# Kernel tuning notes

Measured on AMD Instinct MI355X. Metric: run time of the kernel, lower is better.

## Reference

```python
import jax, jax.numpy as jnp
import numpy as np

HEAD_SIZE = 64   # baseChn * max_channel_ratio
NUM_HEADS = 2
LEAKY_ALPHA = 0.3  # tf.keras.layers.LeakyReLU default


def setup_inputs() -> dict:
    key = jax.random.key(0)
    ks = jax.random.split(key, 6)
    x = jax.random.normal(ks[0], (96, 48, 512), dtype=jnp.float32)
    y = jax.random.uniform(ks[1], (96, 64, 64), dtype=jnp.float32)
    nItem = jax.random.uniform(ks[2], (96,), dtype=jnp.float32, minval=1.0, maxval=48.0)
    W_proj = jax.random.normal(ks[3], (512, 64), dtype=jnp.float32) * 0.05
    W1 = jax.random.normal(ks[4], (64, 128), dtype=jnp.float32) * 0.1
    W2 = jax.random.normal(ks[5], (2, 1), dtype=jnp.float32)
    return {"x": x, "y": y, "nItem": nItem, "W_proj": W_proj, "W1": W1, "W2": W2}


def reference(x, y, nItem, W_proj, W1, W2):
    # fc_cnn_proj: Dense(64, gelu exact, no bias)
    gallery = jax.nn.gelu(jnp.matmul(x, W_proj), approximate=False)  # [Sx, Nx, 64]
    Sx, Nx, _ = gallery.shape
    Sy, Ny, _ = y.shape
    sqrt_hs = jnp.sqrt(jnp.float32(HEAD_SIZE))
    # shared linear (no bias) then split heads: [S, H, N, hs]
    px = jnp.matmul(gallery, W1).reshape(Sx, Nx, NUM_HEADS, HEAD_SIZE).transpose(0, 2, 1, 3)
    py = jnp.matmul(y, W1).reshape(Sy, Ny, NUM_HEADS, HEAD_SIZE).transpose(0, 2, 1, 3)
    # pairwise cross-set attention maps: [Sy, Sx, H, Ny, Nx]
    att = jnp.einsum('yhmd,xhnd->yxhmn', py, px) / sqrt_hs
    att = jnp.where(att > 0, att, LEAKY_ALPHA * att)
    # reduce over both item axes, normalize by nItem[x] and nItemMax_y
    sc = att.sum(axis=(3, 4)) / nItem[None, :, None] / jnp.float32(Ny)  # [Sy, Sx, H]
    scores = jnp.matmul(sc, W2)  # linear2: Dense(1, no bias) -> [Sy, Sx, 1]
    return scores
```

## Files before the change

### kernel.cpp

```cpp
#include <hip/hip_runtime.h>
#include <hip/hip_bf16.h>


typedef short bf16x8 __attribute__((ext_vector_type(8)));
typedef float f32x4 __attribute__((ext_vector_type(4)));

__device__ __forceinline__ unsigned short f2bf(float v) {
  __hip_bfloat16 b = __float2bfloat16(v);
  return *reinterpret_cast<unsigned short*>(&b);
}

__device__ __forceinline__ bf16x8 load8_cvt(const float* __restrict__ p) {
  f32x4 v0 = *reinterpret_cast<const f32x4*>(p);
  f32x4 v1 = *reinterpret_cast<const f32x4*>(p + 4);
  bf16x8 r;
  r[0] = (short)f2bf(v0[0]); r[1] = (short)f2bf(v0[1]);
  r[2] = (short)f2bf(v0[2]); r[3] = (short)f2bf(v0[3]);
  r[4] = (short)f2bf(v1[0]); r[5] = (short)f2bf(v1[1]);
  r[6] = (short)f2bf(v1[2]); r[7] = (short)f2bf(v1[3]);
  return r;
}

__global__ __launch_bounds__(256) void k_wprep(const float* __restrict__ Wp,
                                               const float* __restrict__ W1,
                                               unsigned short* __restrict__ WpF,
                                               unsigned short* __restrict__ W1F) {
  int tid = blockIdx.x * 256 + threadIdx.x;
  if (tid < 32768) {
    int kc = tid >> 11, nt = (tid >> 9) & 3, l = (tid >> 3) & 63, i = tid & 7;
    int k = 32 * kc + 8 * (l >> 4) + i, c = nt * 16 + (l & 15);
    WpF[tid] = f2bf(Wp[k * 64 + c]);
  } else {
    int t2 = tid - 32768;
    int kc = t2 >> 12, nt = (t2 >> 9) & 7, l = (t2 >> 3) & 63, i = t2 & 7;
    int k = 32 * kc + 8 * (l >> 4) + i, d = nt * 16 + (l & 15);
    W1F[t2] = f2bf(W1[k * 128 + d]);
  }
}

__global__ __launch_bounds__(256) void k_py(const float* __restrict__ y,
                                            const unsigned short* __restrict__ W1F_u,
                                            unsigned short* __restrict__ pyf) {
  int lane = threadIdx.x & 63;
  int w = threadIdx.x >> 6;
  int T = blockIdx.x * 4 + w;
  const bf16x8* W1F = reinterpret_cast<const bf16x8*>(W1F_u);
  const float* yb = y + (size_t)(T * 16 + (lane & 15)) * 64 + 8 * (lane >> 4);
  bf16x8 a0 = load8_cvt(yb);
  bf16x8 a1 = load8_cvt(yb + 32);
  f32x4 acc[8];
#pragma unroll
  for (int nt = 0; nt < 8; ++nt) acc[nt] = (f32x4){0.f, 0.f, 0.f, 0.f};
#pragma unroll
  for (int nt = 0; nt < 8; ++nt) {
    acc[nt] = __builtin_amdgcn_mfma_f32_16x16x32_bf16(a0, W1F[nt * 64 + lane], acc[nt], 0, 0, 0);
    acc[nt] = __builtin_amdgcn_mfma_f32_16x16x32_bf16(a1, W1F[(8 + nt) * 64 + lane], acc[nt], 0, 0, 0);
  }
  int r_hi = (lane >> 4) * 4;
#pragma unroll
  for (int nt = 0; nt < 8; ++nt) {
    int d = nt * 16 + (lane & 15);
    int h = d >> 6, dd = d & 63;
    int kc = dd >> 5, q = (dd >> 3) & 3, i = dd & 7;
#pragma unroll
    for (int j = 0; j < 4; ++j) {
      int row = T * 16 + r_hi + j;
      int yi = row >> 6, m = row & 63;
      int mt = m >> 4, rr = m & 15;
      size_t idx = ((size_t)((yi * 2 + h) * 8 + mt * 2 + kc)) * 512 + (rr + (q << 4)) * 8 + i;
      pyf[idx] = f2bf(acc[nt][j]);
    }
  }
}

__global__ __launch_bounds__(256) void k_gal_px(const float* __restrict__ x,
                                                const unsigned short* __restrict__ WpF_u,
                                                const unsigned short* __restrict__ W1F_u,
                                                unsigned short* __restrict__ pxf) {
  __shared__ float red[4 * 16 * 64];
  __shared__ unsigned short gal[16 * 72];
  int lane = threadIdx.x & 63;
  int w = threadIdx.x >> 6;
  int rowbase = blockIdx.x * 16;
  const bf16x8* WpF = reinterpret_cast<const bf16x8*>(WpF_u);
  const bf16x8* W1F = reinterpret_cast<const bf16x8*>(W1F_u);
  const float* xb = x + (size_t)(rowbase + (lane & 15)) * 512 + 8 * (lane >> 4);

  f32x4 acc1[4];
#pragma unroll
  for (int nt = 0; nt < 4; ++nt) acc1[nt] = (f32x4){0.f, 0.f, 0.f, 0.f};
#pragma unroll
  for (int kk = 0; kk < 4; ++kk) {
    int kc = w * 4 + kk;
    bf16x8 a = load8_cvt(xb + 32 * kc);
#pragma unroll
    for (int nt = 0; nt < 4; ++nt)
      acc1[nt] = __builtin_amdgcn_mfma_f32_16x16x32_bf16(a, WpF[(kc * 4 + nt) * 64 + lane], acc1[nt], 0, 0, 0);
  }
#pragma unroll
  for (int nt = 0; nt < 4; ++nt)
#pragma unroll
    for (int j = 0; j < 4; ++j)
      red[(w * 16 + nt * 4 + j) * 64 + lane] = acc1[nt][j];
  __syncthreads();
#pragma unroll
  for (int j = 0; j < 4; ++j) {
    float s = red[(0 * 16 + w * 4 + j) * 64 + lane] + red[(1 * 16 + w * 4 + j) * 64 + lane]
            + red[(2 * 16 + w * 4 + j) * 64 + lane] + red[(3 * 16 + w * 4 + j) * 64 + lane];
    float ge = 0.5f * s * (1.0f + erff(s * 0.70710678118654752f));
    int r = (lane >> 4) * 4 + j;
    int c = w * 16 + (lane & 15);
    gal[r * 72 + c] = f2bf(ge);
  }
  __syncthreads();
  const unsigned short* gp = &gal[(lane & 15) * 72 + 8 * (lane >> 4)];
  bf16x8 g0 = *reinterpret_cast<const bf16x8*>(gp);
  bf16x8 g1 = *reinterpret_cast<const bf16x8*>(gp + 32);
  f32x4 acc2[2];
  acc2[0] = (f32x4){0.f, 0.f, 0.f, 0.f};
  acc2[1] = (f32x4){0.f, 0.f, 0.f, 0.f};
#pragma unroll
  for (int u = 0; u < 2; ++u) {
    int nt = w * 2 + u;
    acc2[u] = __builtin_amdgcn_mfma_f32_16x16x32_bf16(g0, W1F[nt * 64 + lane], acc2[u], 0, 0, 0);
    acc2[u] = __builtin_amdgcn_mfma_f32_16x16x32_bf16(g1, W1F[(8 + nt) * 64 + lane], acc2[u], 0, 0, 0);
  }
#pragma unroll
  for (int u = 0; u < 2; ++u) {
    int nt = w * 2 + u;
    int d = nt * 16 + (lane & 15);
    int h = d >> 6, dd = d & 63;
    int kc = dd >> 5, q = (dd >> 3) & 3, i = dd & 7;
#pragma unroll
    for (int j = 0; j < 4; ++j) {
      int row = rowbase + (lane >> 4) * 4 + j;
      int xi = row / 48, n = row % 48;
      int nt3 = n >> 4, rr = n & 15;
      size_t idx = ((size_t)((xi * 2 + h) * 6 + nt3 * 2 + kc)) * 512 + (rr + (q << 4)) * 8 + i;
      pxf[idx] = f2bf(acc2[u][j]);
    }
  }
}

__global__ __launch_bounds__(256) void k_att(const unsigned short* __restrict__ pyf_u,
                                             const unsigned short* __restrict__ pxf_u,
                                             const float* __restrict__ nItem,
                                             const float* __restrict__ W2,
                                             float* __restrict__ out) {
  int lane = threadIdx.x & 63;
  int w = threadIdx.x >> 6;
  int yi = blockIdx.x / 6;
  int xib = (blockIdx.x % 6) * 16 + w * 4;
  const bf16x8* PA = reinterpret_cast<const bf16x8*>(pyf_u);
  const bf16x8* PB = reinterpret_cast<const bf16x8*>(pxf_u);
  float sv[4][2];
#pragma unroll
  for (int g = 0; g < 4; ++g) { sv[g][0] = 0.f; sv[g][1] = 0.f; }
#pragma unroll
  for (int h = 0; h < 2; ++h) {
    bf16x8 a[4][2];
    size_t ab = (size_t)(yi * 2 + h) * 512 + lane;
#pragma unroll
    for (int mt = 0; mt < 4; ++mt) {
      a[mt][0] = PA[ab + (mt * 2 + 0) * 64];
      a[mt][1] = PA[ab + (mt * 2 + 1) * 64];
    }
#pragma unroll
    for (int g = 0; g < 4; ++g) {
      size_t bb = (size_t)((xib + g) * 2 + h) * 384 + lane;
      bf16x8 b[3][2];
#pragma unroll
      for (int nt = 0; nt < 3; ++nt) {
        b[nt][0] = PB[bb + (nt * 2 + 0) * 64];
        b[nt][1] = PB[bb + (nt * 2 + 1) * 64];
      }
      float sz = 0.f, sr = 0.f;
#pragma unroll
      for (int nt = 0; nt < 3; ++nt)
#pragma unroll
        for (int mt = 0; mt < 4; ++mt) {
          f32x4 acc = {0.f, 0.f, 0.f, 0.f};
          acc = __builtin_amdgcn_mfma_f32_16x16x32_bf16(a[mt][0], b[nt][0], acc, 0, 0, 0);
          acc = __builtin_amdgcn_mfma_f32_16x16x32_bf16(a[mt][1], b[nt][1], acc, 0, 0, 0);
#pragma unroll
          for (int j = 0; j < 4; ++j) { sz += acc[j]; sr += fmaxf(acc[j], 0.f); }
        }
      sv[g][h] += 0.3f * sz + 0.7f * sr;
    }
  }
#pragma unroll
  for (int g = 0; g < 4; ++g)
#pragma unroll
    for (int h = 0; h < 2; ++h)
#pragma unroll
      for (int off = 32; off >= 1; off >>= 1)
        sv[g][h] += __shfl_xor(sv[g][h], off, 64);
  if (lane == 0) {
    float w2a = W2[0], w2b = W2[1];
#pragma unroll
    for (int g = 0; g < 4; ++g) {
      int xi = xib + g;
      out[yi * 96 + xi] = (sv[g][0] * w2a + sv[g][1] * w2b) / (512.0f * nItem[xi]);
    }
  }
}

extern "C" void kernel_launch(void* const* d_in, const int* in_sizes, int n_in,
                              void* d_out, int out_size, void* d_ws, size_t ws_size,
                              hipStream_t stream) {
  const float* x     = (const float*)d_in[0];
  const float* y     = (const float*)d_in[1];
  const float* nItem = (const float*)d_in[2];
  const float* Wp    = (const float*)d_in[3];
  const float* W1    = (const float*)d_in[4];
  const float* W2    = (const float*)d_in[5];
  float* out = (float*)d_out;

  unsigned short* WpF = (unsigned short*)d_ws;
  unsigned short* W1F = WpF + 32768;
  unsigned short* pyf = W1F + 8192;
  unsigned short* pxf = pyf + 786432;

  hipLaunchKernelGGL(k_wprep, dim3(160), dim3(256), 0, stream, Wp, W1, WpF, W1F);
  hipLaunchKernelGGL(k_py, dim3(96), dim3(256), 0, stream, y, W1F, pyf);
  hipLaunchKernelGGL(k_gal_px, dim3(288), dim3(256), 0, stream, x, WpF, W1F, pxf);
  hipLaunchKernelGGL(k_att, dim3(576), dim3(256), 0, stream, pyf, pxf, nItem, W2, out);
}
```

Baseline: 40.81 us.

## Fuse weight prep, py and gallery/px projections into one kernel; restructure attention

Merges the weight-reformatting, py projection and gallery/px projection kernels into a single launch. Each block converts W1 and W_proj to bf16 fragment layout in shared memory, so the separate prep kernel and its global round-trip go away. Each wave now runs the full K=512 gallery GEMM itself instead of reducing partial sums across waves through LDS. The attention kernel is remapped so each wave owns one y-row with all of its A fragments held in registers, and W2 and the leaky-ReLU constants are folded into vector accumulators. The cost is that every block repeats the weight conversion, and there are fewer, heavier blocks (72 for x).

New measurement: 34.89 us. 14.5% less time.

```diff
diff --git a/kernel.cpp b/kernel.cpp
--- a/kernel.cpp
+++ b/kernel.cpp
@@ -21,123 +21,134 @@
   return r;
 }
 
-__global__ __launch_bounds__(256) void k_wprep(const float* __restrict__ Wp,
-                                               const float* __restrict__ W1,
-                                               unsigned short* __restrict__ WpF,
-                                               unsigned short* __restrict__ W1F) {
-  int tid = blockIdx.x * 256 + threadIdx.x;
-  if (tid < 32768) {
-    int kc = tid >> 11, nt = (tid >> 9) & 3, l = (tid >> 3) & 63, i = tid & 7;
-    int k = 32 * kc + 8 * (l >> 4) + i, c = nt * 16 + (l & 15);
-    WpF[tid] = f2bf(Wp[k * 64 + c]);
+__global__ __launch_bounds__(256) void k_prep(const float* __restrict__ x,
+                                              const float* __restrict__ y,
+                                              const float* __restrict__ Wp,
+                                              const float* __restrict__ W1,
+                                              unsigned short* __restrict__ pyf,
+                                              unsigned short* __restrict__ pxf) {
+  __shared__ unsigned short w1f[8192];
+  __shared__ unsigned short wpf[16384];
+  __shared__ unsigned short gal[4][1152];
+  int t = threadIdx.x;
+  int lane = t & 63, w = t >> 6;
+
+#pragma unroll
+  for (int it = 0; it < 32; ++it) {
+    int idx = it * 256 + t;
+    int k = idx >> 7, d = idx & 127;
+    int l = (d & 15) + 16 * ((k >> 3) & 3);
+    int f = (k >> 5) * 8 + (d >> 4);
+    w1f[f * 512 + l * 8 + (k & 7)] = f2bf(W1[idx]);
+  }
+
+  if (blockIdx.x >= 72) {
+    __syncthreads();
+    int yi = blockIdx.x - 72;
+    const bf16x8* WF = reinterpret_cast<const bf16x8*>(w1f);
+    int row0 = yi * 64 + w * 16 + (lane & 15);
+    const float* yb = y + (size_t)row0 * 64 + 8 * (lane >> 4);
+    bf16x8 a0 = load8_cvt(yb);
+    bf16x8 a1 = load8_cvt(yb + 32);
+    f32x4 acc[8];
+#pragma unroll
+    for (int nt = 0; nt < 8; ++nt) acc[nt] = (f32x4){0.f, 0.f, 0.f, 0.f};
+#pragma unroll
+    for (int nt = 0; nt < 8; ++nt) {
+      acc[nt] = __builtin_amdgcn_mfma_f32_16x16x32_bf16(a0, WF[nt * 64 + lane], acc[nt], 0, 0, 0);
+      acc[nt] = __builtin_amdgcn_mfma_f32_16x16x32_bf16(a1, WF[(8 + nt) * 64 + lane], acc[nt], 0, 0, 0);
+    }
+    int r_hi = (lane >> 4) * 4;
+#pragma unroll
+    for (int nt = 0; nt < 8; ++nt) {
+      int d = nt * 16 + (lane & 15);
+      int h = d >> 6, dd = d & 63;
+      int kc = dd >> 5, q = (dd >> 3) & 3, i = dd & 7;
+#pragma unroll
+      for (int j = 0; j < 4; ++j) {
+        int m = w * 16 + r_hi + j;
+        int mt = m >> 4, rr = m & 15;
+        size_t idx = ((size_t)((yi * 2 + h) * 8 + mt * 2 + kc)) * 512 + (rr + (q << 4)) * 8 + i;
+        pyf[idx] = f2bf(acc[nt][j]);
+      }
+    }
   } else {
-    int t2 = tid - 32768;
-    int kc = t2 >> 12, nt = (t2 >> 9) & 7, l = (t2 >> 3) & 63, i = t2 & 7;
-    int k = 32 * kc + 8 * (l >> 4) + i, d = nt * 16 + (l & 15);
-    W1F[t2] = f2bf(W1[k * 128 + d]);
-  }
-}
-
-__global__ __launch_bounds__(256) void k_py(const float* __restrict__ y,
-                                            const unsigned short* __restrict__ W1F_u,
-                                            unsigned short* __restrict__ pyf) {
-  int lane = threadIdx.x & 63;
-  int w = threadIdx.x >> 6;
-  int T = blockIdx.x * 4 + w;
-  const bf16x8* W1F = reinterpret_cast<const bf16x8*>(W1F_u);
-  const float* yb = y + (size_t)(T * 16 + (lane & 15)) * 64 + 8 * (lane >> 4);
-  bf16x8 a0 = load8_cvt(yb);
-  bf16x8 a1 = load8_cvt(yb + 32);
-  f32x4 acc[8];
-#pragma unroll
-  for (int nt = 0; nt < 8; ++nt) acc[nt] = (f32x4){0.f, 0.f, 0.f, 0.f};
-#pragma unroll
-  for (int nt = 0; nt < 8; ++nt) {
-    acc[nt] = __builtin_amdgcn_mfma_f32_16x16x32_bf16(a0, W1F[nt * 64 + lane], acc[nt], 0, 0, 0);
-    acc[nt] = __builtin_amdgcn_mfma_f32_16x16x32_bf16(a1, W1F[(8 + nt) * 64 + lane], acc[nt], 0, 0, 0);
-  }
-  int r_hi = (lane >> 4) * 4;
-#pragma unroll
-  for (int nt = 0; nt < 8; ++nt) {
-    int d = nt * 16 + (lane & 15);
-    int h = d >> 6, dd = d & 63;
-    int kc = dd >> 5, q = (dd >> 3) & 3, i = dd & 7;
-#pragma unroll
-    for (int j = 0; j < 4; ++j) {
-      int row = T * 16 + r_hi + j;
-      int yi = row >> 6, m = row & 63;
-      int mt = m >> 4, rr = m & 15;
-      size_t idx = ((size_t)((yi * 2 + h) * 8 + mt * 2 + kc)) * 512 + (rr + (q << 4)) * 8 + i;
-      pyf[idx] = f2bf(acc[nt][j]);
-    }
-  }
-}
-
-__global__ __launch_bounds__(256) void k_gal_px(const float* __restrict__ x,
-                                                const unsigned short* __restrict__ WpF_u,
-                                                const unsigned short* __restrict__ W1F_u,
-                                                unsigned short* __restrict__ pxf) {
-  __shared__ float red[4 * 16 * 64];
-  __shared__ unsigned short gal[16 * 72];
-  int lane = threadIdx.x & 63;
-  int w = threadIdx.x >> 6;
-  int rowbase = blockIdx.x * 16;
-  const bf16x8* WpF = reinterpret_cast<const bf16x8*>(WpF_u);
-  const bf16x8* W1F = reinterpret_cast<const bf16x8*>(W1F_u);
-  const float* xb = x + (size_t)(rowbase + (lane & 15)) * 512 + 8 * (lane >> 4);
-
-  f32x4 acc1[4];
-#pragma unroll
-  for (int nt = 0; nt < 4; ++nt) acc1[nt] = (f32x4){0.f, 0.f, 0.f, 0.f};
-#pragma unroll
-  for (int kk = 0; kk < 4; ++kk) {
-    int kc = w * 4 + kk;
-    bf16x8 a = load8_cvt(xb + 32 * kc);
+    int rowbase = blockIdx.x * 64;
+#pragma unroll
+    for (int it = 0; it < 64; ++it) {
+      int idx = it * 256 + t;
+      int k = idx >> 6, c = idx & 63;
+      int l = (c & 15) + 16 * ((k >> 3) & 3);
+      int g = ((k >> 5) & 7) * 4 + (c >> 4);
+      wpf[g * 512 + l * 8 + (k & 7)] = f2bf(Wp[idx]);
+    }
+    __syncthreads();
+    const bf16x8* WPF = reinterpret_cast<const bf16x8*>(wpf);
+    const bf16x8* WF = reinterpret_cast<const bf16x8*>(w1f);
+    int rloc = rowbase + w * 16 + (lane & 15);
+    const float* xb = x + (size_t)rloc * 512 + 8 * (lane >> 4);
+    f32x4 acc1[4];
+#pragma unroll
+    for (int nt = 0; nt < 4; ++nt) acc1[nt] = (f32x4){0.f, 0.f, 0.f, 0.f};
+#pragma unroll
+    for (int kc = 0; kc < 8; ++kc) {
+      bf16x8 a = load8_cvt(xb + 32 * kc);
+#pragma unroll
+      for (int nt = 0; nt < 4; ++nt)
+        acc1[nt] = __builtin_amdgcn_mfma_f32_16x16x32_bf16(a, WPF[(kc * 4 + nt) * 64 + lane], acc1[nt], 0, 0, 0);
+    }
+    __syncthreads();
+#pragma unroll
+    for (int it = 0; it < 64; ++it) {
+      int idx = it * 256 + t;
+      int k = idx >> 6, c = idx & 63;
+      int l = (c & 15) + 16 * ((k >> 3) & 3);
+      int g = ((k >> 5) & 7) * 4 + (c >> 4);
+      wpf[g * 512 + l * 8 + (k & 7)] = f2bf(Wp[16384 + idx]);
+    }
+    __syncthreads();
+#pragma unroll
+    for (int kc = 0; kc < 8; ++kc) {
+      bf16x8 a = load8_cvt(xb + 256 + 32 * kc);
+#pragma unroll
+      for (int nt = 0; nt < 4; ++nt)
+        acc1[nt] = __builtin_amdgcn_mfma_f32_16x16x32_bf16(a, WPF[(kc * 4 + nt) * 64 + lane], acc1[nt], 0, 0, 0);
+    }
 #pragma unroll
     for (int nt = 0; nt < 4; ++nt)
-      acc1[nt] = __builtin_amdgcn_mfma_f32_16x16x32_bf16(a, WpF[(kc * 4 + nt) * 64 + lane], acc1[nt], 0, 0, 0);
-  }
-#pragma unroll
-  for (int nt = 0; nt < 4; ++nt)
-#pragma unroll
-    for (int j = 0; j < 4; ++j)
-      red[(w * 16 + nt * 4 + j) * 64 + lane] = acc1[nt][j];
-  __syncthreads();
-#pragma unroll
-  for (int j = 0; j < 4; ++j) {
-    float s = red[(0 * 16 + w * 4 + j) * 64 + lane] + red[(1 * 16 + w * 4 + j) * 64 + lane]
-            + red[(2 * 16 + w * 4 + j) * 64 + lane] + red[(3 * 16 + w * 4 + j) * 64 + lane];
-    float ge = 0.5f * s * (1.0f + erff(s * 0.70710678118654752f));
-    int r = (lane >> 4) * 4 + j;
-    int c = w * 16 + (lane & 15);
-    gal[r * 72 + c] = f2bf(ge);
-  }
-  __syncthreads();
-  const unsigned short* gp = &gal[(lane & 15) * 72 + 8 * (lane >> 4)];
-  bf16x8 g0 = *reinterpret_cast<const bf16x8*>(gp);
-  bf16x8 g1 = *reinterpret_cast<const bf16x8*>(gp + 32);
-  f32x4 acc2[2];
-  acc2[0] = (f32x4){0.f, 0.f, 0.f, 0.f};
-  acc2[1] = (f32x4){0.f, 0.f, 0.f, 0.f};
-#pragma unroll
-  for (int u = 0; u < 2; ++u) {
-    int nt = w * 2 + u;
-    acc2[u] = __builtin_amdgcn_mfma_f32_16x16x32_bf16(g0, W1F[nt * 64 + lane], acc2[u], 0, 0, 0);
-    acc2[u] = __builtin_amdgcn_mfma_f32_16x16x32_bf16(g1, W1F[(8 + nt) * 64 + lane], acc2[u], 0, 0, 0);
-  }
-#pragma unroll
-  for (int u = 0; u < 2; ++u) {
-    int nt = w * 2 + u;
-    int d = nt * 16 + (lane & 15);
-    int h = d >> 6, dd = d & 63;
-    int kc = dd >> 5, q = (dd >> 3) & 3, i = dd & 7;
-#pragma unroll
-    for (int j = 0; j < 4; ++j) {
-      int row = rowbase + (lane >> 4) * 4 + j;
-      int xi = row / 48, n = row % 48;
-      int nt3 = n >> 4, rr = n & 15;
-      size_t idx = ((size_t)((xi * 2 + h) * 6 + nt3 * 2 + kc)) * 512 + (rr + (q << 4)) * 8 + i;
-      pxf[idx] = f2bf(acc2[u][j]);
+#pragma unroll
+      for (int j = 0; j < 4; ++j) {
+        float s = acc1[nt][j];
+        float ge = 0.5f * s * (1.0f + erff(s * 0.70710678118654752f));
+        int rl = (lane >> 4) * 4 + j;
+        int c = nt * 16 + (lane & 15);
+        gal[w][rl * 72 + c] = f2bf(ge);
+      }
+    const unsigned short* gp = &gal[w][(lane & 15) * 72 + 8 * (lane >> 4)];
+    bf16x8 g0 = *reinterpret_cast<const bf16x8*>(gp);
+    bf16x8 g1 = *reinterpret_cast<const bf16x8*>(gp + 32);
+    f32x4 acc2[8];
+#pragma unroll
+    for (int nt = 0; nt < 8; ++nt) acc2[nt] = (f32x4){0.f, 0.f, 0.f, 0.f};
+#pragma unroll
+    for (int nt = 0; nt < 8; ++nt) {
+      acc2[nt] = __builtin_amdgcn_mfma_f32_16x16x32_bf16(g0, WF[nt * 64 + lane], acc2[nt], 0, 0, 0);
+      acc2[nt] = __builtin_amdgcn_mfma_f32_16x16x32_bf16(g1, WF[(8 + nt) * 64 + lane], acc2[nt], 0, 0, 0);
+    }
+    int r_hi = (lane >> 4) * 4;
+#pragma unroll
+    for (int nt = 0; nt < 8; ++nt) {
+      int d = nt * 16 + (lane & 15);
+      int h = d >> 6, dd = d & 63;
+      int kc = dd >> 5, q = (dd >> 3) & 3, i = dd & 7;
+#pragma unroll
+      for (int j = 0; j < 4; ++j) {
+        int row = rowbase + w * 16 + r_hi + j;
+        int xi = row / 48, n = row % 48;
+        int nt3 = n >> 4, rr = n & 15;
+        size_t idx = ((size_t)((xi * 2 + h) * 6 + nt3 * 2 + kc)) * 512 + (rr + (q << 4)) * 8 + i;
+        pxf[idx] = f2bf(acc2[nt][j]);
+      }
     }
   }
 }
@@ -149,58 +160,58 @@
                                              float* __restrict__ out) {
   int lane = threadIdx.x & 63;
   int w = threadIdx.x >> 6;
-  int yi = blockIdx.x / 6;
-  int xib = (blockIdx.x % 6) * 16 + w * 4;
+  int yi = (blockIdx.x / 24) * 4 + w;
+  int xb = (blockIdx.x % 24) * 4;
   const bf16x8* PA = reinterpret_cast<const bf16x8*>(pyf_u);
   const bf16x8* PB = reinterpret_cast<const bf16x8*>(pxf_u);
-  float sv[4][2];
-#pragma unroll
-  for (int g = 0; g < 4; ++g) { sv[g][0] = 0.f; sv[g][1] = 0.f; }
-#pragma unroll
-  for (int h = 0; h < 2; ++h) {
-    bf16x8 a[4][2];
-    size_t ab = (size_t)(yi * 2 + h) * 512 + lane;
-#pragma unroll
-    for (int mt = 0; mt < 4; ++mt) {
-      a[mt][0] = PA[ab + (mt * 2 + 0) * 64];
-      a[mt][1] = PA[ab + (mt * 2 + 1) * 64];
-    }
+
+  f32x4 zero4 = {0.f, 0.f, 0.f, 0.f};
+  asm volatile("" : "+v"(zero4));
+
+  bf16x8 a[16];
+  size_t abase = (size_t)(yi * 2) * 512 + lane;
+#pragma unroll
+  for (int f = 0; f < 8; ++f) {
+    a[f]     = PA[abase + f * 64];
+    a[8 + f] = PA[abase + 512 + f * 64];
+  }
+  float w2h0 = W2[0], w2h1 = W2[1];
+  float res[4];
+#pragma unroll
+  for (int g = 0; g < 4; ++g) {
+    int xi = xb + g;
+    f32x4 szw = {0.f, 0.f, 0.f, 0.f};
+    f32x4 srw = {0.f, 0.f, 0.f, 0.f};
+#pragma unroll
+    for (int h = 0; h < 2; ++h) {
+      size_t bbase = (size_t)((xi * 2 + h) * 6) * 64 + lane;
+      bf16x8 b[6];
+#pragma unroll
+      for (int f = 0; f < 6; ++f) b[f] = PB[bbase + f * 64];
+      float c3 = 0.3f * (h ? w2h1 : w2h0);
+      float c7 = 0.7f * (h ? w2h1 : w2h0);
+#pragma unroll
+      for (int nt = 0; nt < 3; ++nt)
+#pragma unroll
+        for (int mt = 0; mt < 4; ++mt) {
+          f32x4 acc = __builtin_amdgcn_mfma_f32_16x16x32_bf16(a[h * 8 + mt * 2], b[nt * 2], zero4, 0, 0, 0);
+          acc = __builtin_amdgcn_mfma_f32_16x16x32_bf16(a[h * 8 + mt * 2 + 1], b[nt * 2 + 1], acc, 0, 0, 0);
+          f32x4 mx = {fmaxf(acc[0], 0.f), fmaxf(acc[1], 0.f), fmaxf(acc[2], 0.f), fmaxf(acc[3], 0.f)};
+          szw += acc * c3;
+          srw += mx * c7;
+        }
+    }
+    f32x4 t4 = szw + srw;
+    float tot = (t4[0] + t4[1]) + (t4[2] + t4[3]);
+#pragma unroll
+    for (int off = 32; off >= 1; off >>= 1) tot += __shfl_xor(tot, off, 64);
+    res[g] = tot;
+  }
+  if (lane == 0) {
 #pragma unroll
     for (int g = 0; g < 4; ++g) {
-      size_t bb = (size_t)((xib + g) * 2 + h) * 384 + lane;
-      bf16x8 b[3][2];
-#pragma unroll
-      for (int nt = 0; nt < 3; ++nt) {
-        b[nt][0] = PB[bb + (nt * 2 + 0) * 64];
-        b[nt][1] = PB[bb + (nt * 2 + 1) * 64];
-      }
-      float sz = 0.f, sr = 0.f;
-#pragma unroll
-      for (int nt = 0; nt < 3; ++nt)
-#pragma unroll
-        for (int mt = 0; mt < 4; ++mt) {
-          f32x4 acc = {0.f, 0.f, 0.f, 0.f};
-          acc = __builtin_amdgcn_mfma_f32_16x16x32_bf16(a[mt][0], b[nt][0], acc, 0, 0, 0);
-          acc = __builtin_amdgcn_mfma_f32_16x16x32_bf16(a[mt][1], b[nt][1], acc, 0, 0, 0);
-#pragma unroll
-          for (int j = 0; j < 4; ++j) { sz += acc[j]; sr += fmaxf(acc[j], 0.f); }
-        }
-      sv[g][h] += 0.3f * sz + 0.7f * sr;
-    }
-  }
-#pragma unroll
-  for (int g = 0; g < 4; ++g)
-#pragma unroll
-    for (int h = 0; h < 2; ++h)
-#pragma unroll
-      for (int off = 32; off >= 1; off >>= 1)
-        sv[g][h] += __shfl_xor(sv[g][h], off, 64);
-  if (lane == 0) {
-    float w2a = W2[0], w2b = W2[1];
-#pragma unroll
-    for (int g = 0; g < 4; ++g) {
-      int xi = xib + g;
-      out[yi * 96 + xi] = (sv[g][0] * w2a + sv[g][1] * w2b) / (512.0f * nItem[xi]);
+      int xi = xb + g;
+      out[yi * 96 + xi] = res[g] / (512.0f * nItem[xi]);
     }
   }
 }
@@ -216,13 +227,9 @@
   const float* W2    = (const float*)d_in[5];
   float* out = (float*)d_out;
 
-  unsigned short* WpF = (unsigned short*)d_ws;
-  unsigned short* W1F = WpF + 32768;
-  unsigned short* pyf = W1F + 8192;
+  unsigned short* pyf = (unsigned short*)d_ws;
   unsigned short* pxf = pyf + 786432;
 
-  hipLaunchKernelGGL(k_wprep, dim3(160), dim3(256), 0, stream, Wp, W1, WpF, W1F);
-  hipLaunchKernelGGL(k_py, dim3(96), dim3(256), 0, stream, y, W1F, pyf);
-  hipLaunchKernelGGL(k_gal_px, dim3(288), dim3(256), 0, stream, x, WpF, W1F, pxf);
+  hipLaunchKernelGGL(k_prep, dim3(168), dim3(256), 0, stream, x, y, Wp, W1, pyf, pxf);
   hipLaunchKernelGGL(k_att, dim3(576), dim3(256), 0, stream, pyf, pxf, nItem, W2, out);
 }
```

## Fuse projection, py/px computation and attention scoring into one mega kernel

Applied to the files above, without the earlier changes.

Replaces the three kernels k_py, k_gal_px and k_att with a single k_mega launched over 1152 blocks. Each block handles 4 y-sets and 2 x-sets. It recomputes the gallery projection, GELU and px for its x-sets, and py for its y-sets, keeping everything in shared memory so the pyf/pxf global round trips and two launches go away. In exchange, gallery/px work is recomputed 24 times over and py work 48 times over, which adds a large amount of redundant MFMA and global x/y reads. Wave utilization is also uneven, since only waves 0-1 handle the second x tile.

Result: slower. 86.97 us (+113.1%).

```diff
diff --git a/kernel.cpp b/kernel.cpp
--- a/kernel.cpp
+++ b/kernel.cpp
@@ -38,170 +38,170 @@
   }
 }
 
-__global__ __launch_bounds__(256) void k_py(const float* __restrict__ y,
-                                            const unsigned short* __restrict__ W1F_u,
-                                            unsigned short* __restrict__ pyf) {
-  int lane = threadIdx.x & 63;
-  int w = threadIdx.x >> 6;
-  int T = blockIdx.x * 4 + w;
-  const bf16x8* W1F = reinterpret_cast<const bf16x8*>(W1F_u);
-  const float* yb = y + (size_t)(T * 16 + (lane & 15)) * 64 + 8 * (lane >> 4);
-  bf16x8 a0 = load8_cvt(yb);
-  bf16x8 a1 = load8_cvt(yb + 32);
-  f32x4 acc[8];
-#pragma unroll
-  for (int nt = 0; nt < 8; ++nt) acc[nt] = (f32x4){0.f, 0.f, 0.f, 0.f};
-#pragma unroll
-  for (int nt = 0; nt < 8; ++nt) {
-    acc[nt] = __builtin_amdgcn_mfma_f32_16x16x32_bf16(a0, W1F[nt * 64 + lane], acc[nt], 0, 0, 0);
-    acc[nt] = __builtin_amdgcn_mfma_f32_16x16x32_bf16(a1, W1F[(8 + nt) * 64 + lane], acc[nt], 0, 0, 0);
-  }
-  int r_hi = (lane >> 4) * 4;
-#pragma unroll
-  for (int nt = 0; nt < 8; ++nt) {
-    int d = nt * 16 + (lane & 15);
-    int h = d >> 6, dd = d & 63;
-    int kc = dd >> 5, q = (dd >> 3) & 3, i = dd & 7;
+__global__ __launch_bounds__(256, 2) void k_mega(const float* __restrict__ x,
+                                                 const float* __restrict__ y,
+                                                 const float* __restrict__ nItem,
+                                                 const float* __restrict__ W2,
+                                                 const unsigned short* __restrict__ WpF_u,
+                                                 const unsigned short* __restrict__ W1F_u,
+                                                 float* __restrict__ out) {
+  __shared__ unsigned short w1f[8192];
+  __shared__ unsigned short wpq[8192];
+  __shared__ unsigned short gal[96 * 72];
+  __shared__ unsigned short pxf[2 * 6 * 512];
+  int t = threadIdx.x;
+  int lane = t & 63, w = t >> 6;
+  int yb = blockIdx.x / 48, xq = blockIdx.x % 48;
+  int yi = yb * 4 + w;
+  int xrow0 = xq * 96;
+  int xi0 = xq * 2;
+
+  float w2h[2] = {W2[0], W2[1]};
+  float nI0 = nItem[xi0], nI1 = nItem[xi0 + 1];
+
+  const bf16x8* WPFg = reinterpret_cast<const bf16x8*>(WpF_u);
+  const bf16x8* W1Fg = reinterpret_cast<const bf16x8*>(W1F_u);
+  const bf16x8* WF = reinterpret_cast<const bf16x8*>(w1f);
+  const bf16x8* WPQ = reinterpret_cast<const bf16x8*>(wpq);
+
+#pragma unroll
+  for (int it = 0; it < 4; ++it)
+    reinterpret_cast<bf16x8*>(w1f)[it * 256 + t] = W1Fg[it * 256 + t];
+
+  int tA = w, tB = 4 + w;
+  f32x4 accA[4], accB[4];
+#pragma unroll
+  for (int nt = 0; nt < 4; ++nt) { accA[nt] = (f32x4){0,0,0,0}; accB[nt] = (f32x4){0,0,0,0}; }
+  const float* xa = x + (size_t)(xrow0 + tA * 16 + (lane & 15)) * 512 + 8 * (lane >> 4);
+  const float* xb2 = x + (size_t)(xrow0 + tB * 16 + (lane & 15)) * 512 + 8 * (lane >> 4);
+#pragma unroll
+  for (int q = 0; q < 4; ++q) {
+    if (q) __syncthreads();
+#pragma unroll
+    for (int it = 0; it < 4; ++it)
+      reinterpret_cast<bf16x8*>(wpq)[it * 256 + t] = WPFg[q * 1024 + it * 256 + t];
+    __syncthreads();
+#pragma unroll
+    for (int kk = 0; kk < 4; ++kk) {
+      int kc = q * 4 + kk;
+      bf16x8 a = load8_cvt(xa + 32 * kc);
+#pragma unroll
+      for (int nt = 0; nt < 4; ++nt)
+        accA[nt] = __builtin_amdgcn_mfma_f32_16x16x32_bf16(a, WPQ[(kk * 4 + nt) * 64 + lane], accA[nt], 0, 0, 0);
+      if (w < 2) {
+        bf16x8 a2 = load8_cvt(xb2 + 32 * kc);
+#pragma unroll
+        for (int nt = 0; nt < 4; ++nt)
+          accB[nt] = __builtin_amdgcn_mfma_f32_16x16x32_bf16(a2, WPQ[(kk * 4 + nt) * 64 + lane], accB[nt], 0, 0, 0);
+      }
+    }
+  }
+#pragma unroll
+  for (int nt = 0; nt < 4; ++nt)
 #pragma unroll
     for (int j = 0; j < 4; ++j) {
-      int row = T * 16 + r_hi + j;
-      int yi = row >> 6, m = row & 63;
-      int mt = m >> 4, rr = m & 15;
-      size_t idx = ((size_t)((yi * 2 + h) * 8 + mt * 2 + kc)) * 512 + (rr + (q << 4)) * 8 + i;
-      pyf[idx] = f2bf(acc[nt][j]);
-    }
-  }
-}
-
-__global__ __launch_bounds__(256) void k_gal_px(const float* __restrict__ x,
-                                                const unsigned short* __restrict__ WpF_u,
-                                                const unsigned short* __restrict__ W1F_u,
-                                                unsigned short* __restrict__ pxf) {
-  __shared__ float red[4 * 16 * 64];
-  __shared__ unsigned short gal[16 * 72];
-  int lane = threadIdx.x & 63;
-  int w = threadIdx.x >> 6;
-  int rowbase = blockIdx.x * 16;
-  const bf16x8* WpF = reinterpret_cast<const bf16x8*>(WpF_u);
-  const bf16x8* W1F = reinterpret_cast<const bf16x8*>(W1F_u);
-  const float* xb = x + (size_t)(rowbase + (lane & 15)) * 512 + 8 * (lane >> 4);
-
-  f32x4 acc1[4];
-#pragma unroll
-  for (int nt = 0; nt < 4; ++nt) acc1[nt] = (f32x4){0.f, 0.f, 0.f, 0.f};
-#pragma unroll
-  for (int kk = 0; kk < 4; ++kk) {
-    int kc = w * 4 + kk;
-    bf16x8 a = load8_cvt(xb + 32 * kc);
-#pragma unroll
-    for (int nt = 0; nt < 4; ++nt)
-      acc1[nt] = __builtin_amdgcn_mfma_f32_16x16x32_bf16(a, WpF[(kc * 4 + nt) * 64 + lane], acc1[nt], 0, 0, 0);
-  }
-#pragma unroll
-  for (int nt = 0; nt < 4; ++nt)
-#pragma unroll
-    for (int j = 0; j < 4; ++j)
-      red[(w * 16 + nt * 4 + j) * 64 + lane] = acc1[nt][j];
+      float s = accA[nt][j];
+      float ge = 0.5f * s * (1.0f + erff(s * 0.70710678118654752f));
+      gal[(tA * 16 + (lane >> 4) * 4 + j) * 72 + nt * 16 + (lane & 15)] = f2bf(ge);
+      if (w < 2) {
+        float s2 = accB[nt][j];
+        float ge2 = 0.5f * s2 * (1.0f + erff(s2 * 0.70710678118654752f));
+        gal[(tB * 16 + (lane >> 4) * 4 + j) * 72 + nt * 16 + (lane & 15)] = f2bf(ge2);
+      }
+    }
   __syncthreads();
-#pragma unroll
-  for (int j = 0; j < 4; ++j) {
-    float s = red[(0 * 16 + w * 4 + j) * 64 + lane] + red[(1 * 16 + w * 4 + j) * 64 + lane]
-            + red[(2 * 16 + w * 4 + j) * 64 + lane] + red[(3 * 16 + w * 4 + j) * 64 + lane];
-    float ge = 0.5f * s * (1.0f + erff(s * 0.70710678118654752f));
-    int r = (lane >> 4) * 4 + j;
-    int c = w * 16 + (lane & 15);
-    gal[r * 72 + c] = f2bf(ge);
-  }
-  __syncthreads();
-  const unsigned short* gp = &gal[(lane & 15) * 72 + 8 * (lane >> 4)];
-  bf16x8 g0 = *reinterpret_cast<const bf16x8*>(gp);
-  bf16x8 g1 = *reinterpret_cast<const bf16x8*>(gp + 32);
-  f32x4 acc2[2];
-  acc2[0] = (f32x4){0.f, 0.f, 0.f, 0.f};
-  acc2[1] = (f32x4){0.f, 0.f, 0.f, 0.f};
-#pragma unroll
-  for (int u = 0; u < 2; ++u) {
-    int nt = w * 2 + u;
-    acc2[u] = __builtin_amdgcn_mfma_f32_16x16x32_bf16(g0, W1F[nt * 64 + lane], acc2[u], 0, 0, 0);
-    acc2[u] = __builtin_amdgcn_mfma_f32_16x16x32_bf16(g1, W1F[(8 + nt) * 64 + lane], acc2[u], 0, 0, 0);
-  }
-#pragma unroll
-  for (int u = 0; u < 2; ++u) {
-    int nt = w * 2 + u;
-    int d = nt * 16 + (lane & 15);
-    int h = d >> 6, dd = d & 63;
-    int kc = dd >> 5, q = (dd >> 3) & 3, i = dd & 7;
-#pragma unroll
-    for (int j = 0; j < 4; ++j) {
-      int row = rowbase + (lane >> 4) * 4 + j;
-      int xi = row / 48, n = row % 48;
-      int nt3 = n >> 4, rr = n & 15;
-      size_t idx = ((size_t)((xi * 2 + h) * 6 + nt3 * 2 + kc)) * 512 + (rr + (q << 4)) * 8 + i;
-      pxf[idx] = f2bf(acc2[u][j]);
-    }
-  }
-}
-
-__global__ __launch_bounds__(256) void k_att(const unsigned short* __restrict__ pyf_u,
-                                             const unsigned short* __restrict__ pxf_u,
-                                             const float* __restrict__ nItem,
-                                             const float* __restrict__ W2,
-                                             float* __restrict__ out) {
-  int lane = threadIdx.x & 63;
-  int w = threadIdx.x >> 6;
-  int yi = blockIdx.x / 6;
-  int xib = (blockIdx.x % 6) * 16 + w * 4;
-  const bf16x8* PA = reinterpret_cast<const bf16x8*>(pyf_u);
-  const bf16x8* PB = reinterpret_cast<const bf16x8*>(pxf_u);
-  float sv[4][2];
-#pragma unroll
-  for (int g = 0; g < 4; ++g) { sv[g][0] = 0.f; sv[g][1] = 0.f; }
+
+  f32x4 zero4 = {0.f, 0.f, 0.f, 0.f};
+  asm volatile("" : "+v"(zero4));
+
+  unsigned short* pyb = wpq + w * 2048;
+  f32x4 res4[2] = {(f32x4){0,0,0,0}, (f32x4){0,0,0,0}};
+
 #pragma unroll
   for (int h = 0; h < 2; ++h) {
-    bf16x8 a[4][2];
-    size_t ab = (size_t)(yi * 2 + h) * 512 + lane;
-#pragma unroll
-    for (int mt = 0; mt < 4; ++mt) {
-      a[mt][0] = PA[ab + (mt * 2 + 0) * 64];
-      a[mt][1] = PA[ab + (mt * 2 + 1) * 64];
-    }
-#pragma unroll
-    for (int g = 0; g < 4; ++g) {
-      size_t bb = (size_t)((xib + g) * 2 + h) * 384 + lane;
-      bf16x8 b[3][2];
-#pragma unroll
-      for (int nt = 0; nt < 3; ++nt) {
-        b[nt][0] = PB[bb + (nt * 2 + 0) * 64];
-        b[nt][1] = PB[bb + (nt * 2 + 1) * 64];
-      }
-      float sz = 0.f, sr = 0.f;
-#pragma unroll
-      for (int nt = 0; nt < 3; ++nt)
+#pragma unroll
+    for (int u = 0; u < 2; ++u) {
+      int tt = u ? tB : tA;
+      if (u && w >= 2) break;
+      const unsigned short* gp = &gal[(tt * 16 + (lane & 15)) * 72 + 8 * (lane >> 4)];
+      bf16x8 g0 = *reinterpret_cast<const bf16x8*>(gp);
+      bf16x8 g1 = *reinterpret_cast<const bf16x8*>(gp + 32);
+#pragma unroll
+      for (int nt = 0; nt < 4; ++nt) {
+        f32x4 acc2 = __builtin_amdgcn_mfma_f32_16x16x32_bf16(g0, WF[(h * 4 + nt) * 64 + lane], zero4, 0, 0, 0);
+        acc2 = __builtin_amdgcn_mfma_f32_16x16x32_bf16(g1, WF[(8 + h * 4 + nt) * 64 + lane], acc2, 0, 0, 0);
+        int dh = nt * 16 + (lane & 15);
+        int kc = dh >> 5, q2 = (dh >> 3) & 3, i = dh & 7;
+#pragma unroll
+        for (int j = 0; j < 4; ++j) {
+          int row = tt * 16 + (lane >> 4) * 4 + j;
+          int xiL = row >= 48;
+          int n = row - 48 * xiL;
+          int nt3 = n >> 4, rr = n & 15;
+          pxf[(xiL * 6 + nt3 * 2 + kc) * 512 + (rr + (q2 << 4)) * 8 + i] = f2bf(acc2[j]);
+        }
+      }
+    }
+    bf16x8 A8h[8];
+#pragma unroll
+    for (int ms = 0; ms < 4; ms += 2) {
+#pragma unroll
+      for (int mm = 0; mm < 2; ++mm) {
+        int mt = ms + mm;
+        const float* ybp = y + (size_t)(yi * 64 + mt * 16 + (lane & 15)) * 64 + 8 * (lane >> 4);
+        bf16x8 a0 = load8_cvt(ybp);
+        bf16x8 a1 = load8_cvt(ybp + 32);
+#pragma unroll
+        for (int nt = 0; nt < 4; ++nt) {
+          f32x4 accp = __builtin_amdgcn_mfma_f32_16x16x32_bf16(a0, WF[(h * 4 + nt) * 64 + lane], zero4, 0, 0, 0);
+          accp = __builtin_amdgcn_mfma_f32_16x16x32_bf16(a1, WF[(8 + h * 4 + nt) * 64 + lane], accp, 0, 0, 0);
+          int dh = nt * 16 + (lane & 15);
+          int kc = dh >> 5, q2 = (dh >> 3) & 3, i = dh & 7;
+#pragma unroll
+          for (int j = 0; j < 4; ++j) {
+            int rr = (lane >> 4) * 4 + j;
+            pyb[(mm * 2 + kc) * 512 + (rr + (q2 << 4)) * 8 + i] = f2bf(accp[j]);
+          }
+        }
+      }
+#pragma unroll
+      for (int mm = 0; mm < 2; ++mm)
+#pragma unroll
+        for (int kc = 0; kc < 2; ++kc)
+          A8h[(ms + mm) * 2 + kc] = *reinterpret_cast<const bf16x8*>(pyb + (mm * 2 + kc) * 512 + lane * 8);
+    }
+    __syncthreads();
+    float c3 = 0.3f * w2h[h], c7 = 0.7f * w2h[h];
+#pragma unroll
+    for (int g = 0; g < 2; ++g) {
+      bf16x8 bb[6];
+#pragma unroll
+      for (int f = 0; f < 6; ++f)
+        bb[f] = *reinterpret_cast<const bf16x8*>(pxf + (g * 6 + f) * 512 + lane * 8);
+#pragma unroll
+      for (int nt3 = 0; nt3 < 3; ++nt3)
 #pragma unroll
         for (int mt = 0; mt < 4; ++mt) {
-          f32x4 acc = {0.f, 0.f, 0.f, 0.f};
-          acc = __builtin_amdgcn_mfma_f32_16x16x32_bf16(a[mt][0], b[nt][0], acc, 0, 0, 0);
-          acc = __builtin_amdgcn_mfma_f32_16x16x32_bf16(a[mt][1], b[nt][1], acc, 0, 0, 0);
-#pragma unroll
-          for (int j = 0; j < 4; ++j) { sz += acc[j]; sr += fmaxf(acc[j], 0.f); }
+          f32x4 acc = __builtin_amdgcn_mfma_f32_16x16x32_bf16(A8h[mt * 2], bb[nt3 * 2], zero4, 0, 0, 0);
+          acc = __builtin_amdgcn_mfma_f32_16x16x32_bf16(A8h[mt * 2 + 1], bb[nt3 * 2 + 1], acc, 0, 0, 0);
+          f32x4 mx = {fmaxf(acc[0], 0.f), fmaxf(acc[1], 0.f), fmaxf(acc[2], 0.f), fmaxf(acc[3], 0.f)};
+          res4[g] += acc * c3;
+          res4[g] += mx * c7;
         }
-      sv[g][h] += 0.3f * sz + 0.7f * sr;
-    }
-  }
-#pragma unroll
-  for (int g = 0; g < 4; ++g)
-#pragma unroll
-    for (int h = 0; h < 2; ++h)
-#pragma unroll
-      for (int off = 32; off >= 1; off >>= 1)
-        sv[g][h] += __shfl_xor(sv[g][h], off, 64);
+    }
+    __syncthreads();
+  }
+
+  float tot0 = (res4[0][0] + res4[0][1]) + (res4[0][2] + res4[0][3]);
+  float tot1 = (res4[1][0] + res4[1][1]) + (res4[1][2] + res4[1][3]);
+#pragma unroll
+  for (int off = 32; off >= 1; off >>= 1) {
+    tot0 += __shfl_xor(tot0, off, 64);
+    tot1 += __shfl_xor(tot1, off, 64);
+  }
   if (lane == 0) {
-    float w2a = W2[0], w2b = W2[1];
-#pragma unroll
-    for (int g = 0; g < 4; ++g) {
-      int xi = xib + g;
-      out[yi * 96 + xi] = (sv[g][0] * w2a + sv[g][1] * w2b) / (512.0f * nItem[xi]);
-    }
+    out[yi * 96 + xi0]     = tot0 / (512.0f * nI0);
+    out[yi * 96 + xi0 + 1] = tot1 / (512.0f * nI1);
   }
 }
 
@@ -218,11 +218,8 @@
 
   unsigned short* WpF = (unsigned short*)d_ws;
   unsigned short* W1F = WpF + 32768;
-  unsigned short* pyf = W1F + 8192;
-  unsigned short* pxf = pyf + 786432;
 
   hipLaunchKernelGGL(k_wprep, dim3(160), dim3(256), 0, stream, Wp, W1, WpF, W1F);
-  hipLaunchKernelGGL(k_py, dim3(96), dim3(256), 0, stream, y, W1F, pyf);
-  hipLaunchKernelGGL(k_gal_px, dim3(288), dim3(256), 0, stream, x, WpF, W1F, pxf);
-  hipLaunchKernelGGL(k_att, dim3(576), dim3(256), 0, stream, pyf, pxf, nItem, W2, out);
-}
+  hipLaunchKernelGGL(k_mega, dim3(1152), dim3(256), 0, stream,
+                     x, y, nItem, W2, WpF, W1F, out);
+}
```
